# Kernel optimization log

Measured on AMD Instinct MI355X. Metric: run time of the kernel, lower is better.

## Reference

```python
import jax, jax.numpy as jnp
import numpy as np

H, W, D = 60, 60, 36            # voxel grid dims (x, y, z)
GRID = 0.08                      # voxel size in meters
SCALE_MULT = 3.0                 # radius multiplier
CHUNK = 7200                     # point-chunk size; 129600 / 7200 = 18 chunks
P = 2048                         # number of Gaussians
C = 13                           # semantic channels


def setup_inputs() -> dict:
    key = jax.random.key(0)
    k1, k2, k3, k4, k5 = jax.random.split(key, 5)
    # query points = voxel centers, guaranteed in-range for the int-bin asserts
    ii, jj, kk = jnp.meshgrid(jnp.arange(H), jnp.arange(W), jnp.arange(D), indexing='ij')
    pts = (jnp.stack([ii, jj, kk], axis=-1).reshape(-1, 3).astype(jnp.float32) + 0.5) * GRID
    pts = pts[None]  # [1, N, 3]
    lo = jnp.array([0.1, 0.1, 0.1], jnp.float32)
    hi = jnp.array([H, W, D], jnp.float32) * GRID - 0.1
    means3D = jax.random.uniform(k1, (1, P, 3), dtype=jnp.float32) * (hi - lo) + lo
    scales = jax.random.uniform(k2, (1, P, 3), minval=0.03, maxval=0.2, dtype=jnp.float32)
    # random rotations via QR -> SPD covariance Sigma = Q diag(s^2) Q^T
    A = jax.random.normal(k3, (P, 3, 3), dtype=jnp.float32)
    Q, _ = jnp.linalg.qr(A)
    cov3D = jnp.einsum('pij,pj,pkj->pik', Q, scales[0] ** 2, Q)[None]  # [1,P,3,3]
    opacities = jax.random.uniform(k4, (1, P), minval=0.1, maxval=1.0, dtype=jnp.float32)
    semantics = jax.random.normal(k5, (1, P, C), dtype=jnp.float32)
    origin_use = jnp.zeros((3,), jnp.float32)
    return {"pts": pts, "means3D": means3D, "opacities": opacities,
            "semantics": semantics, "scales": scales, "cov3D": cov3D,
            "origin_use": origin_use}


def _sym_inv6(packed):
    # packed: [P,6] = (xx, yy, zz, xy, yz, xz) of a symmetric 3x3 covariance
    a, b, c, d, e, f = (packed[:, i] for i in range(6))
    det = a * (b * c - e * e) - d * (d * c - e * f) + f * (d * e - b * f)
    ixx = (b * c - e * e) / det
    iyy = (a * c - f * f) / det
    izz = (a * b - d * d) / det
    ixy = (e * f - d * c) / det
    iyz = (d * f - a * e) / det
    ixz = (d * e - b * f) / det
    return ixx, iyy, izz, ixy, iyz, ixz


def _forward(pts, means3D, opacities, semantics, scales, cov3D, origin_use):
    pts = pts[0]                    # [N,3], no grad in original
    means3D = means3D[0]            # [P,3]
    opacities = opacities[0]        # [P]
    semantics = semantics[0]        # [P,C]
    scales = jax.lax.stop_gradient(scales[0])   # detached in original
    cov3D = cov3D[0]                # [P,3,3]

    radii = jnp.ceil(scales.max(-1) * SCALE_MULT / GRID).astype(jnp.int32)  # [P]
    m_int = ((jax.lax.stop_gradient(means3D) - origin_use) / GRID).astype(jnp.int32)  # [P,3]
    packed = cov3D.reshape(-1, 9)[:, jnp.array([0, 4, 8, 1, 5, 2])]  # [P,6]
    ixx, iyy, izz, ixy, iyz, ixz = _sym_inv6(packed)  # per-Gaussian inverse cov entries

    N = pts.shape[0]
    pts_c = pts.reshape(N // CHUNK, CHUNK, 3)

    def chunk_fn(p):  # p: [CHUNK,3]
        p_int = ((p - origin_use) / GRID).astype(jnp.int32)
        dx = p[:, 0:1] - means3D[None, :, 0]   # [CHUNK,P]
        dy = p[:, 1:2] - means3D[None, :, 1]
        dz = p[:, 2:3] - means3D[None, :, 2]
        quad = (ixx * dx * dx + iyy * dy * dy + izz * dz * dz
                + 2.0 * (ixy * dx * dy + iyz * dy * dz + ixz * dx * dz))
        inbox = (jnp.abs(p_int[:, None, :] - m_int[None, :, :])
                 <= radii[None, :, None]).all(-1)          # [CHUNK,P] box/bin test
        w = jnp.where(inbox, opacities[None, :] * jnp.exp(-0.5 * quad), 0.0)
        return w @ semantics                                # [CHUNK,C]

    logits = jax.lax.map(chunk_fn, pts_c).reshape(N, C)
    return logits


def reference(pts, means3D, opacities, semantics, scales, cov3D, origin_use):
    return _forward(pts, means3D, opacities, semantics, scales, cov3D, origin_use)
```

## Files before the change

### kernel.cpp

```cpp
#include <hip/hip_runtime.h>


constexpr int   HH      = 60;
constexpr int   WW      = 60;
constexpr int   DD      = 36;
constexpr int   P_N     = 2048;
constexpr int   C_N     = 13;
constexpr int   REC     = 24;
constexpr int   BXD     = 15;
constexpr int   BYD     = 15;
constexpr int   BZD     = 9;
constexpr int   NBRICK  = BXD * BYD * BZD;
constexpr int   MAXL    = 256;
constexpr float GRID_SZ = 0.08f;

__global__ void precompute_kernel(const float* __restrict__ means,
                                  const float* __restrict__ opac,
                                  const float* __restrict__ sem,
                                  const float* __restrict__ scales,
                                  const float* __restrict__ cov,
                                  const float* __restrict__ origin,
                                  float* __restrict__ recs,
                                  int4* __restrict__ boxes) {
    int g = blockIdx.x * blockDim.x + threadIdx.x;
    if (g >= P_N) return;
    float mx = means[g * 3 + 0], my = means[g * 3 + 1], mz = means[g * 3 + 2];
    float sx = scales[g * 3 + 0], sy = scales[g * 3 + 1], sz = scales[g * 3 + 2];
    float smax = fmaxf(sx, fmaxf(sy, sz));
    int rad = (int)ceilf(smax * 3.0f / GRID_SZ);
    float ox = origin[0], oy = origin[1], oz = origin[2];
    int mix = (int)((mx - ox) / GRID_SZ);
    int miy = (int)((my - oy) / GRID_SZ);
    int miz = (int)((mz - oz) / GRID_SZ);
    const float* cv = cov + g * 9;
    float a = cv[0], b = cv[4], c = cv[8], d = cv[1], e = cv[5], f = cv[2];
    float det = a * (b * c - e * e) - d * (d * c - e * f) + f * (d * e - b * f);
    const float kD = -0.5f * 1.44269504088896340736f;
    const float kO = -1.44269504088896340736f;
    float* r = recs + g * REC;
    r[0] = mx; r[1] = my; r[2] = mz;
    r[3] = __log2f(opac[g]);
    r[4] = kD * (b * c - e * e) / det;
    r[5] = kD * (a * c - f * f) / det;
    r[6] = kD * (a * b - d * d) / det;
    r[7] = kO * (e * f - d * c) / det;
    r[8] = kO * (d * f - a * e) / det;
    r[9] = kO * (d * e - b * f) / det;
#pragma unroll
    for (int cc = 0; cc < C_N; ++cc) r[10 + cc] = sem[g * C_N + cc];
    r[23] = 0.0f;
    boxes[g] = make_int4(mix, miy, miz, rad);
}

__global__ __launch_bounds__(256) void agg_kernel(const float* __restrict__ recs,
                                                  const int4* __restrict__ boxes,
                                                  float* __restrict__ out) {
    __shared__ int   s_idx[MAXL];
    __shared__ int   s_cnt;
    __shared__ float s_acc[4][64][C_N];

    const int b = (int)blockIdx.x;
    const int bk = b % BZD; const int rem = b / BZD;
    const int bj = rem % BYD; const int bi = rem / BYD;
    const int i0 = bi * 4, j0 = bj * 4, k0 = bk * 4;

    if (threadIdx.x == 0) s_cnt = 0;
    __syncthreads();

    for (int g = (int)threadIdx.x; g < P_N; g += 256) {
        int4 bx = boxes[g];
        bool ov = (bx.x - bx.w <= i0 + 3) && (bx.x + bx.w >= i0)
               && (bx.y - bx.w <= j0 + 3) && (bx.y + bx.w >= j0)
               && (bx.z - bx.w <= k0 + 3) && (bx.z + bx.w >= k0);
        if (ov) {
            int xlo = max(bx.x - bx.w - i0, 0), xhi = min(bx.x + bx.w - i0, 3);
            int ylo = max(bx.y - bx.w - j0, 0), yhi = min(bx.y + bx.w - j0, 3);
            int zlo = max(bx.z - bx.w - k0, 0), zhi = min(bx.z + bx.w - k0, 3);
            unsigned mx4 = (0xFu >> (3 - xhi)) & (0xFu << xlo);
            unsigned my4 = (0xFu >> (3 - yhi)) & (0xFu << ylo);
            unsigned mz4 = (0xFu >> (3 - zhi)) & (0xFu << zlo);
            unsigned ent = (unsigned)g | (mx4 << 12) | (my4 << 16) | (mz4 << 20);
            int t = atomicAdd(&s_cnt, 1);
            if (t < MAXL) s_idx[t] = (int)ent;
        }
    }
    __syncthreads();
    const int cnt = min(s_cnt, MAXL);

    const int wave = (int)threadIdx.x >> 6;
    const int lane = (int)threadIdx.x & 63;
    const int kk = lane & 3, lj = (lane >> 2) & 3, li = lane >> 4;
    const int gi = i0 + li, gj = j0 + lj, k = k0 + kk;
    const float px = ((float)gi + 0.5f) * GRID_SZ;
    const float py = ((float)gj + 0.5f) * GRID_SZ;
    const float pz = ((float)k  + 0.5f) * GRID_SZ;
    const unsigned sel = (1u << (12 + li)) | (1u << (16 + lj)) | (1u << (20 + kk));

    float acc[C_N];
#pragma unroll
    for (int cc = 0; cc < C_N; ++cc) acc[cc] = 0.0f;

#pragma unroll 2
    for (int i = wave; i < cnt; i += 4) {
        const unsigned ent = (unsigned)__builtin_amdgcn_readfirstlane(s_idx[i]);
        const int g = (int)(ent & 0xFFFu);
        const float* __restrict__ r = recs + (long)g * REC;
        const bool inbox = (ent & sel) == sel;
        const float dx = px - r[0], dy = py - r[1], dz = pz - r[2];
        float e2 = r[3];
        e2 = fmaf(r[4], dx * dx, e2);
        e2 = fmaf(r[5], dy * dy, e2);
        e2 = fmaf(r[6], dz * dz, e2);
        e2 = fmaf(r[7], dx * dy, e2);
        e2 = fmaf(r[8], dy * dz, e2);
        e2 = fmaf(r[9], dx * dz, e2);
        float w = exp2f(e2);
        w = inbox ? w : 0.0f;
#pragma unroll
        for (int cc = 0; cc < C_N; ++cc)
            acc[cc] = fmaf(w, r[10 + cc], acc[cc]);
    }

#pragma unroll
    for (int cc = 0; cc < C_N; ++cc) s_acc[wave][lane][cc] = acc[cc];
    __syncthreads();

    for (int t = (int)threadIdx.x; t < 64 * C_N; t += 256) {
        const int v = t / C_N, c = t % C_N;
        const float s = s_acc[0][v][c] + s_acc[1][v][c]
                      + s_acc[2][v][c] + s_acc[3][v][c];
        const int vk = v & 3, vj = (v >> 2) & 3, vi = v >> 4;
        const long n = (long)(i0 + vi) * (WW * DD)
                     + (long)(j0 + vj) * DD + (k0 + vk);
        out[n * C_N + c] = s;
    }
}

extern "C" void kernel_launch(void* const* d_in, const int* in_sizes, int n_in,
                              void* d_out, int out_size, void* d_ws, size_t ws_size,
                              hipStream_t stream) {
    const float* means  = (const float*)d_in[1];
    const float* opac   = (const float*)d_in[2];
    const float* sem    = (const float*)d_in[3];
    const float* scales = (const float*)d_in[4];
    const float* cov    = (const float*)d_in[5];
    const float* origin = (const float*)d_in[6];
    float* out = (float*)d_out;

    char* ws = (char*)d_ws;
    float* recs  = (float*)ws;
    int4*  boxes = (int4*)(ws + 196608);

    precompute_kernel<<<(P_N + 255) / 256, 256, 0, stream>>>(
        means, opac, sem, scales, cov, origin, recs, boxes);
    agg_kernel<<<NBRICK, 256, 0, stream>>>(recs, boxes, out);
}
```

Measured before the change: 86.23 us.

## Split aggregation into cull/gather and eval kernels with contiguous per-brick streams

Splits the brick aggregation into two kernels. The first culls Gaussians per brick and copies their records, with the packed mask entry stored in the pad slot, into a contiguous per-brick stream in workspace. The second kernel evaluates from that stream, giving each wave a contiguous quarter of the list, and uses the hardware exp2 builtin. The aim is to replace scattered indexed record loads with sequential reads, at the cost of an extra launch and a workspace write and re-read of the gathered records.

```diff
diff --git a/kernel.cpp b/kernel.cpp
--- a/kernel.cpp
+++ b/kernel.cpp
@@ -52,12 +52,12 @@
     boxes[g] = make_int4(mix, miy, miz, rad);
 }
 
-__global__ __launch_bounds__(256) void agg_kernel(const float* __restrict__ recs,
-                                                  const int4* __restrict__ boxes,
-                                                  float* __restrict__ out) {
-    __shared__ int   s_idx[MAXL];
-    __shared__ int   s_cnt;
-    __shared__ float s_acc[4][64][C_N];
+__global__ __launch_bounds__(256) void cull_gather(const float* __restrict__ recs,
+                                                   const int4* __restrict__ boxes,
+                                                   float* __restrict__ streams,
+                                                   int* __restrict__ counts) {
+    __shared__ int s_idx[MAXL];
+    __shared__ int s_cnt;
 
     const int b = (int)blockIdx.x;
     const int bk = b % BZD; const int rem = b / BZD;
@@ -86,6 +86,28 @@
     }
     __syncthreads();
     const int cnt = min(s_cnt, MAXL);
+    if (threadIdx.x == 0) counts[b] = cnt;
+
+    float4* dst = (float4*)(streams + (long)b * MAXL * REC);
+    for (int t = (int)threadIdx.x; t < cnt * 6; t += 256) {
+        const int e = t / 6, part = t % 6;
+        const int ent = s_idx[e];
+        const int g = ent & 0xFFF;
+        float4 v = ((const float4*)(recs + (long)g * REC))[part];
+        if (part == 5) v.w = __int_as_float(ent);
+        dst[e * 6 + part] = v;
+    }
+}
+
+__global__ __launch_bounds__(256) void agg_eval(const float* __restrict__ streams,
+                                                const int* __restrict__ counts,
+                                                float* __restrict__ out) {
+    __shared__ float s_acc[4][64][C_N];
+
+    const int b = (int)blockIdx.x;
+    const int bk = b % BZD; const int rem = b / BZD;
+    const int bj = rem % BYD; const int bi = rem / BYD;
+    const int i0 = bi * 4, j0 = bj * 4, k0 = bk * 4;
 
     const int wave = (int)threadIdx.x >> 6;
     const int lane = (int)threadIdx.x & 63;
@@ -96,15 +118,19 @@
     const float pz = ((float)k  + 0.5f) * GRID_SZ;
     const unsigned sel = (1u << (12 + li)) | (1u << (16 + lj)) | (1u << (20 + kk));
 
+    const int cnt = counts[b];
+    const int q0 = __builtin_amdgcn_readfirstlane((cnt * wave) >> 2);
+    const int q1 = __builtin_amdgcn_readfirstlane((cnt * (wave + 1)) >> 2);
+    const float* __restrict__ base = streams + (long)b * MAXL * REC;
+
     float acc[C_N];
 #pragma unroll
     for (int cc = 0; cc < C_N; ++cc) acc[cc] = 0.0f;
 
 #pragma unroll 2
-    for (int i = wave; i < cnt; i += 4) {
-        const unsigned ent = (unsigned)__builtin_amdgcn_readfirstlane(s_idx[i]);
-        const int g = (int)(ent & 0xFFFu);
-        const float* __restrict__ r = recs + (long)g * REC;
+    for (int i = q0; i < q1; ++i) {
+        const float* __restrict__ r = base + i * REC;
+        const unsigned ent = (unsigned)__float_as_int(r[23]);
         const bool inbox = (ent & sel) == sel;
         const float dx = px - r[0], dy = py - r[1], dz = pz - r[2];
         float e2 = r[3];
@@ -114,7 +140,7 @@
         e2 = fmaf(r[7], dx * dy, e2);
         e2 = fmaf(r[8], dy * dz, e2);
         e2 = fmaf(r[9], dx * dz, e2);
-        float w = exp2f(e2);
+        float w = __builtin_amdgcn_exp2f(e2);
         w = inbox ? w : 0.0f;
 #pragma unroll
         for (int cc = 0; cc < C_N; ++cc)
@@ -148,10 +174,13 @@
     float* out = (float*)d_out;
 
     char* ws = (char*)d_ws;
-    float* recs  = (float*)ws;
-    int4*  boxes = (int4*)(ws + 196608);
+    float* recs    = (float*)ws;
+    int4*  boxes   = (int4*)(ws + 196608);
+    int*   counts  = (int*)(ws + 196608 + 32768);
+    float* streams = (float*)(ws + 196608 + 32768 + 8192);
 
     precompute_kernel<<<(P_N + 255) / 256, 256, 0, stream>>>(
         means, opac, sem, scales, cov, origin, recs, boxes);
-    agg_kernel<<<NBRICK, 256, 0, stream>>>(recs, boxes, out);
+    cull_gather<<<NBRICK, 256, 0, stream>>>(recs, boxes, streams, counts);
+    agg_eval<<<NBRICK, 256, 0, stream>>>(streams, counts, out);
 }
```

Measured after the change: 94.15 us. +9.2%, slower.
